# Performance work log

Measured on AMD Instinct MI355X. Metric: run time of the kernel, lower is better.

## Reference

```python
import jax, jax.numpy as jnp
import numpy as np

B, S, IN_DIM, P_DIM, H = 2, 2048, 1024, 512, 8
HD = P_DIM // H
N_PENTA = 1024
SCALES = (128, 256, 512)
K_NEIGH = max(16, min(int(S * 0.15), 128))  # adaptive window -> 128
SCALE = 1.0 / float(np.sqrt(HD))
EPS = 1e-5


def _ln(x, g, b):
    mu = jnp.mean(x, axis=-1, keepdims=True)
    var = jnp.mean((x - mu) ** 2, axis=-1, keepdims=True)
    return (x - mu) * jax.lax.rsqrt(var + EPS) * g + b


def setup_inputs() -> dict:
    key = jax.random.key(0)
    ks = list(jax.random.split(key, 6 + 2 * len(SCALES)))
    w = lambda k, shp: jax.random.normal(k, shp, jnp.float32) * 0.02
    inp = {
        'sequence_features': jax.random.normal(ks[0], (B, S, IN_DIM), jnp.float32),
        'shared_pentachora': jax.random.normal(ks[1], (N_PENTA, 5, P_DIM), jnp.float32),
        'shared_positions': jax.random.uniform(ks[2], (N_PENTA,), dtype=jnp.float32),
        'proj_W': w(ks[3], (IN_DIM, P_DIM)), 'proj_b': jnp.zeros((P_DIM,), jnp.float32),
        'ln_g': jnp.ones((P_DIM,), jnp.float32), 'ln_b': jnp.zeros((P_DIM,), jnp.float32),
        'qkv_W': w(ks[4], (P_DIM, 3 * P_DIM)), 'qkv_b': jnp.zeros((3 * P_DIM,), jnp.float32),
        'out_W': w(ks[5], (P_DIM, P_DIM)), 'out_b': jnp.zeros((P_DIM,), jnp.float32),
    }
    i = 6
    for s in SCALES:
        inp[f'w1_{s}'] = w(ks[i], (P_DIM, 2 * s)); inp[f'b1_{s}'] = jnp.zeros((2 * s,), jnp.float32)
        inp[f'g_{s}'] = jnp.ones((2 * s,), jnp.float32); inp[f'bb_{s}'] = jnp.zeros((2 * s,), jnp.float32)
        inp[f'w2_{s}'] = w(ks[i + 1], (2 * s, s)); inp[f'b2_{s}'] = jnp.zeros((s,), jnp.float32)
        i += 2
    return inp


def _attend_one(z_b, pos_b, qkv_W, qkv_b, out_W, out_b):
    # z_b: [S, P_DIM], pos_b: [S]
    qkv = (z_b @ qkv_W + qkv_b).reshape(S, 3, H, HD)
    q = jnp.transpose(qkv[:, 0], (1, 0, 2))  # [H, S, HD]
    k = jnp.transpose(qkv[:, 1], (1, 0, 2))
    v = jnp.transpose(qkv[:, 2], (1, 0, 2))
    dist = jnp.abs(pos_b[:, None] - pos_b[None, :])  # [S, S]
    _, routes = jax.lax.top_k(-dist, K_NEIGH)        # [S, K] nearest in Cantor space
    kg = k[:, routes, :]  # [H, S, K, HD] gathered keys
    vg = v[:, routes, :]
    scores = jnp.einsum('hqd,hqkd->hqk', q, kg) * SCALE
    attn = jax.nn.softmax(scores, axis=-1)
    out = jnp.einsum('hqk,hqkd->hqd', attn, vg)
    out = jnp.transpose(out, (1, 0, 2)).reshape(S, P_DIM)
    return out @ out_W + out_b


def reference(sequence_features, shared_pentachora, shared_positions, proj_W, proj_b, ln_g, ln_b, qkv_W, qkv_b, out_W, out_b, w1_128, b1_128, g_128, bb_128, w2_128, b2_128, w1_256, b1_256, g_256, bb_256, w2_256, b2_256, w1_512, b1_512, g_512, bb_512, w2_512, b2_512):
    # centroids from pentachora vertices, L2-normalized
    cent = shared_pentachora.mean(axis=1)
    cent = cent / jnp.clip(jnp.linalg.norm(cent, axis=-1, keepdims=True), 1e-12)
    # input projection -> LN -> GELU -> L2 normalize
    z = jax.nn.gelu(_ln(sequence_features @ proj_W + proj_b, ln_g, ln_b), approximate=False)
    z = z / jnp.clip(jnp.linalg.norm(z, axis=-1, keepdims=True), 1e-12)
    # match to opinion anchors, inherit Cantor positions
    anchor_ids = jnp.argmax(jnp.einsum('bnd,pd->bnp', z, cent), axis=-1)  # [B, S]
    cantor_positions = shared_positions[anchor_ids]  # [B, S]
    # per-sample geometric sparse attention (vmapped over batch)
    z_att = jax.vmap(_attend_one, in_axes=(0, 0, None, None, None, None))(
        z, cantor_positions, qkv_W, qkv_b, out_W, out_b)  # [B, S, P_DIM]
    pooled = z_att.mean(axis=1)  # [B, P_DIM] (no attention mask)
    scale_params = (
        (w1_128, b1_128, g_128, bb_128, w2_128, b2_128),
        (w1_256, b1_256, g_256, bb_256, w2_256, b2_256),
        (w1_512, b1_512, g_512, bb_512, w2_512, b2_512),
    )
    outs = []
    for (w1, b1, g, bb, w2, b2) in scale_params:
        h = jax.nn.gelu(_ln(pooled @ w1 + b1, g, bb), approximate=False)
        outs.append(h @ w2 + b2)
    return jnp.concatenate(outs, axis=-1)  # [B, 128+256+512] concatenated scale opinions
```

## Files before the change

kernel.cpp:

```cpp
#include <hip/hip_runtime.h>
#include <math.h>

#define DEV __device__ __forceinline__

static constexpr int S_LEN  = 2048;
static constexpr int IN_DIM = 1024;
static constexpr int P_DIM  = 512;
static constexpr int NHEAD  = 8;
static constexpr int HD     = 64;
static constexpr int KN     = 128;

typedef __attribute__((ext_vector_type(8))) short bf16x8;
typedef __attribute__((ext_vector_type(4))) float f32x4;

DEV float gelu_exact(float x) {
    return 0.5f * x * (1.0f + erff(x * 0.70710678118654752440f));
}

DEV short bf_hi(float x) {
    unsigned u = __float_as_uint(x);
    unsigned r = (u + 0x7fffu + ((u >> 16) & 1u)) >> 16;
    return (short)r;
}
DEV float bf_f(short h) { return __uint_as_float(((unsigned)(unsigned short)h) << 16); }

DEV float block_reduce_sum(float v, float* sm4) {
    #pragma unroll
    for (int off = 32; off; off >>= 1) v += __shfl_down(v, off, 64);
    int lane = threadIdx.x & 63, w = threadIdx.x >> 6;
    __syncthreads();
    if (lane == 0) sm4[w] = v;
    __syncthreads();
    return sm4[0] + sm4[1] + sm4[2] + sm4[3];
}

DEV float wave_sum(float v) {
    #pragma unroll
    for (int off = 32; off; off >>= 1) v += __shfl_xor(v, off, 64);
    return v;
}

DEV void wt_body(const float* __restrict__ W, short* __restrict__ WTh,
                 short* __restrict__ WTl, int K, int N, int bk, int bn,
                 float (*tile)[65]) {
    int t = threadIdx.x;
    int c = t & 63, r4 = t >> 6;
    #pragma unroll
    for (int i = 0; i < 16; i++) {
        int row = r4 + i * 4;
        tile[row][c] = W[(long)(bk * 64 + row) * N + bn * 64 + c];
    }
    __syncthreads();
    #pragma unroll
    for (int i = 0; i < 16; i++) {
        int n = r4 + i * 4;
        float v = tile[c][n];
        short h = bf_hi(v);
        long o = (long)(bn * 64 + n) * K + bk * 64 + c;
        WTh[o] = h;
        WTl[o] = bf_hi(v - bf_f(h));
    }
}

DEV void t32_body(const float* __restrict__ W, float* __restrict__ WT,
                  int K, int N, int bk, int bn, float (*tile)[65]) {
    int t = threadIdx.x;
    int c = t & 63, r4 = t >> 6;
    #pragma unroll
    for (int i = 0; i < 16; i++) {
        int row = r4 + i * 4;
        tile[row][c] = W[(long)(bk * 64 + row) * N + bn * 64 + c];
    }
    __syncthreads();
    #pragma unroll
    for (int i = 0; i < 16; i++) {
        int n = r4 + i * 4;
        WT[(long)(bn * 64 + n) * K + bk * 64 + c] = tile[c][n];
    }
}

__global__ __launch_bounds__(256) void k_prep(const float* __restrict__ penta,
                                              short* __restrict__ ch, short* __restrict__ cl,
                                              const float* __restrict__ projW,
                                              short* __restrict__ pjh, short* __restrict__ pjl,
                                              const float* __restrict__ qkvW,
                                              short* __restrict__ qkh, short* __restrict__ qkl,
                                              const float* __restrict__ seq,
                                              short* __restrict__ sh, short* __restrict__ sl,
                                              unsigned long long* __restrict__ rowkey,
                                              float* __restrict__ pooledZ,
                                              const float* __restrict__ outW, float* __restrict__ outWT,
                                              const float* __restrict__ w1_0,
                                              const float* __restrict__ w1_1,
                                              const float* __restrict__ w1_2, float* __restrict__ w1T,
                                              const float* __restrict__ w2_0,
                                              const float* __restrict__ w2_1,
                                              const float* __restrict__ w2_2, float* __restrict__ w2T) {
    __shared__ float tile[64][65];
    __shared__ float sm4[4];
    int blk = blockIdx.x, t = threadIdx.x;
    if (blk < 1024) {
        int p = blk;
        if (t < 4) rowkey[p * 4 + t] = 0ull;
        if (p < 4) pooledZ[p * 256 + t] = 0.f;
        float c0 = 0.f, c1 = 0.f;
        #pragma unroll
        for (int v = 0; v < 5; v++) {
            const float* row = penta + ((long)p * 5 + v) * P_DIM;
            c0 += row[t];
            c1 += row[t + 256];
        }
        c0 /= 5.0f; c1 /= 5.0f;
        float tot = block_reduce_sum(c0 * c0 + c1 * c1, sm4);
        float n = fmaxf(sqrtf(tot), 1e-12f);
        float v0 = c0 / n, v1 = c1 / n;
        short h0 = bf_hi(v0), h1 = bf_hi(v1);
        ch[p * P_DIM + t]       = h0;
        ch[p * P_DIM + t + 256] = h1;
        cl[p * P_DIM + t]       = bf_hi(v0 - bf_f(h0));
        cl[p * P_DIM + t + 256] = bf_hi(v1 - bf_f(h1));
    } else if (blk < 1152) {
        int id = blk - 1024;
        wt_body(projW, pjh, pjl, IN_DIM, P_DIM, id & 15, id >> 4, tile);
    } else if (blk < 1344) {
        int id = blk - 1152;
        wt_body(qkvW, qkh, qkl, P_DIM, 3 * P_DIM, id & 7, id >> 3, tile);
    } else if (blk < 2368) {
        long base = ((long)(blk - 1344) * 256 + t) * 16;
        #pragma unroll
        for (int u = 0; u < 4; u++) {
            float4 v = *(const float4*)(seq + base + u * 4);
            short h0 = bf_hi(v.x), h1 = bf_hi(v.y), h2 = bf_hi(v.z), h3 = bf_hi(v.w);
            *(short4*)(sh + base + u * 4) = make_short4(h0, h1, h2, h3);
            *(short4*)(sl + base + u * 4) =
                make_short4(bf_hi(v.x - bf_f(h0)), bf_hi(v.y - bf_f(h1)),
                            bf_hi(v.z - bf_f(h2)), bf_hi(v.w - bf_f(h3)));
        }
    } else if (blk < 2432) {
        int id = blk - 2368;
        t32_body(outW, outWT, 512, 512, id & 7, id >> 3, tile);
    } else if (blk < 2464) {
        int id = blk - 2432;
        t32_body(w1_0, w1T, 512, 256, id & 7, id >> 3, tile);
    } else if (blk < 2528) {
        int id = blk - 2464;
        t32_body(w1_1, w1T + 256 * 512, 512, 512, id & 7, id >> 3, tile);
    } else if (blk < 2656) {
        int id = blk - 2528;
        t32_body(w1_2, w1T + 768 * 512, 512, 1024, id & 7, id >> 3, tile);
    } else if (blk < 2664) {
        int id = blk - 2656;
        t32_body(w2_0, w2T, 256, 128, id & 3, id >> 2, tile);
    } else if (blk < 2696) {
        int id = blk - 2664;
        t32_body(w2_1, w2T + 32768, 512, 256, id & 7, id >> 3, tile);
    } else {
        int id = blk - 2696;
        t32_body(w2_2, w2T + 163840, 1024, 512, id & 15, id >> 4, tile);
    }
}

template <int BM, int K, int N, int EPI>
__global__ __launch_bounds__(256) void k_mm(const short* __restrict__ Ash,
                                            const short* __restrict__ Asl,
                                            const short* __restrict__ BTh,
                                            const short* __restrict__ BTl,
                                            const float* __restrict__ bias,
                                            float* __restrict__ C,
                                            unsigned long long* __restrict__ rowkey) {
    constexpr int TI  = BM / 32;
    constexpr int CA  = BM / 8;
    constexpr int NCH = 2 * CA + 32;
    __shared__ __align__(128) short AhS[BM * 64], AlS[BM * 64];
    __shared__ __align__(128) short BhS[128 * 64], BlS[128 * 64];
    int t = threadIdx.x;
    int lane = t & 63, wave = t >> 6;
    int wr = (wave >> 1) * (BM / 2), wc = (wave & 1) * 64;
    int m = lane & 15, quad = lane >> 4;
    int rb = blockIdx.x * BM, cb = blockIdx.y * 128;
    int r8 = lane >> 3, p8 = lane & 7;
    int sl = p8 ^ r8;

    f32x4 acc[TI][4];
    #pragma unroll
    for (int i = 0; i < TI; i++)
        #pragma unroll
        for (int j = 0; j < 4; j++) acc[i][j] = (f32x4){0.f, 0.f, 0.f, 0.f};

    for (int k0 = 0; k0 < K; k0 += 64) {
        __syncthreads();
        for (int c = wave; c < NCH; c += 4) {
            const short* src; short* dst;
            if (c < CA) {
                src = Ash + (long)(rb + c * 8 + r8) * K + k0 + sl * 8;
                dst = AhS + c * 512;
            } else if (c < 2 * CA) {
                int cc = c - CA;
                src = Asl + (long)(rb + cc * 8 + r8) * K + k0 + sl * 8;
                dst = AlS + cc * 512;
            } else if (c < 2 * CA + 16) {
                int cc = c - 2 * CA;
                src = BTh + (long)(cb + cc * 8 + r8) * K + k0 + sl * 8;
                dst = BhS + cc * 512;
            } else {
                int cc = c - 2 * CA - 16;
                src = BTl + (long)(cb + cc * 8 + r8) * K + k0 + sl * 8;
                dst = BlS + cc * 512;
            }
            __builtin_amdgcn_global_load_lds(
                (const __attribute__((address_space(1))) unsigned int*)src,
                (__attribute__((address_space(3))) unsigned int*)dst, 16, 0, 0);
        }
        __syncthreads();

        #pragma unroll
        for (int ks = 0; ks < 2; ks++) {
            int so = ((ks * 4 + quad) ^ (m & 7)) * 8;
            bf16x8 ah[TI], al[TI], bh[4], bl[4];
            #pragma unroll
            for (int i = 0; i < TI; i++) {
                int off = (wr + i * 16 + m) * 64 + so;
                ah[i] = *(const bf16x8*)(AhS + off);
                al[i] = *(const bf16x8*)(AlS + off);
            }
            #pragma unroll
            for (int j = 0; j < 4; j++) {
                int off = (wc + j * 16 + m) * 64 + so;
                bh[j] = *(const bf16x8*)(BhS + off);
                bl[j] = *(const bf16x8*)(BlS + off);
            }
            #pragma unroll
            for (int i = 0; i < TI; i++)
                #pragma unroll
                for (int j = 0; j < 4; j++) {
                    acc[i][j] = __builtin_amdgcn_mfma_f32_16x16x32_bf16(ah[i], bh[j], acc[i][j], 0, 0, 0);
                    acc[i][j] = __builtin_amdgcn_mfma_f32_16x16x32_bf16(ah[i], bl[j], acc[i][j], 0, 0, 0);
                    acc[i][j] = __builtin_amdgcn_mfma_f32_16x16x32_bf16(al[i], bh[j], acc[i][j], 0, 0, 0);
                }
        }
    }

    if (EPI == 0) {
        #pragma unroll
        for (int i = 0; i < TI; i++) {
            int gr0 = rb + wr + i * 16 + quad * 4;
            #pragma unroll
            for (int j = 0; j < 4; j++) {
                int gc = cb + wc + j * 16 + m;
                float bv = bias[gc];
                #pragma unroll
                for (int r = 0; r < 4; r++)
                    C[(long)(gr0 + r) * N + gc] = acc[i][j][r] + bv;
            }
        }
    } else {
        #pragma unroll
        for (int i = 0; i < TI; i++) {
            #pragma unroll
            for (int r = 0; r < 4; r++) {
                int gr = rb + wr + i * 16 + quad * 4 + r;
                float bv = acc[i][0][r];
                int bp = cb + wc + m;
                #pragma unroll
                for (int j = 1; j < 4; j++) {
                    float v = acc[i][j][r];
                    int p = cb + wc + j * 16 + m;
                    if (v > bv) { bv = v; bp = p; }
                }
                #pragma unroll
                for (int off = 1; off < 16; off <<= 1) {
                    float ov = __shfl_xor(bv, off, 64);
                    int op = __shfl_xor(bp, off, 64);
                    if (ov > bv || (ov == bv && op < bp)) { bv = ov; bp = op; }
                }
                if (m == 0) {
                    unsigned u = __float_as_uint(bv);
                    u = (u & 0x80000000u) ? ~u : (u | 0x80000000u);
                    unsigned long long key =
                        ((unsigned long long)u << 32) | (unsigned)(0xFFFFFFFFu - (unsigned)bp);
                    atomicMax(&rowkey[gr], key);
                }
            }
        }
    }
}

__global__ __launch_bounds__(256) void k_ln_gelu_norm(const float* __restrict__ Zin,
                                                      const float* __restrict__ g,
                                                      const float* __restrict__ b,
                                                      short* __restrict__ z_h,
                                                      short* __restrict__ z_l) {
    long row = blockIdx.x;
    int t = threadIdx.x;
    __shared__ float sm4[4];
    float x0 = Zin[row * P_DIM + t], x1 = Zin[row * P_DIM + t + 256];
    float mu = block_reduce_sum(x0 + x1, sm4) * (1.0f / P_DIM);
    float d0 = x0 - mu, d1 = x1 - mu;
    float var = block_reduce_sum(d0 * d0 + d1 * d1, sm4) * (1.0f / P_DIM);
    float rs = 1.0f / sqrtf(var + 1e-5f);
    float y0 = gelu_exact(d0 * rs * g[t] + b[t]);
    float y1 = gelu_exact(d1 * rs * g[t + 256] + b[t + 256]);
    float nn = block_reduce_sum(y0 * y0 + y1 * y1, sm4);
    float n = fmaxf(sqrtf(nn), 1e-12f);
    float v0 = y0 / n, v1 = y1 / n;
    short h0 = bf_hi(v0), h1 = bf_hi(v1);
    z_h[row * P_DIM + t]       = h0;
    z_h[row * P_DIM + t + 256] = h1;
    z_l[row * P_DIM + t]       = bf_hi(v0 - bf_f(h0));
    z_l[row * P_DIM + t + 256] = bf_hi(v1 - bf_f(h1));
}

__global__ __launch_bounds__(256) void k_rank(const unsigned long long* __restrict__ rowkey,
                                              const float* __restrict__ spos,
                                              int* __restrict__ order,
                                              float* __restrict__ pos_srt) {
    int b = blockIdx.y, t = threadIdx.x;
    __shared__ unsigned long long key[2048];
    for (int u = 0; u < 8; u++) {
        int i = t + u * 256;
        unsigned p = 0xFFFFFFFFu - (unsigned)(rowkey[b * 2048 + i] & 0xFFFFFFFFull);
        key[i] = (((unsigned long long)__float_as_uint(spos[p])) << 32) | (unsigned)i;
    }
    __syncthreads();
    int i = blockIdx.x * 256 + t;
    unsigned long long ki = key[i];
    int rank = 0;
    #pragma unroll 8
    for (int j = 0; j < 2048; j++) rank += (key[j] < ki) ? 1 : 0;
    order[b * 2048 + rank]   = i;
    pos_srt[b * 2048 + rank] = __uint_as_float((unsigned)(ki >> 32));
}

__global__ __launch_bounds__(256) void k_routes(const float* __restrict__ pos_srt,
                                                const int* __restrict__ order,
                                                unsigned long long* __restrict__ bmG,
                                                uint2* __restrict__ bounds) {
    int blk = blockIdx.x;
    int b = blk >> 9;
    int t = threadIdx.x;
    int lane = t & 63, wave = t >> 6;
    int r = (blk & 511) * 4 + wave;
    __shared__ float ps[2048];
    __shared__ unsigned short tk[2048];
    for (int u = 0; u < 8; u++) {
        int i = t + u * 256;
        ps[i] = pos_srt[b * 2048 + i];
        tk[i] = (unsigned short)order[b * 2048 + i];
    }
    __syncthreads();

    float pi = ps[r];
    float T = 3e38f;
    #pragma unroll
    for (int a2 = 0; a2 < 2; a2++) {
        int a = lane + a2 * 64;
        int jl = r - a, jr = r + 127 - a;
        if (jl >= 0 && jr <= 2047) {
            float dl = (a > 0)   ? (pi - ps[jl]) : 0.f;
            float dr = (a < 127) ? (ps[jr] - pi) : 0.f;
            T = fminf(T, fmaxf(dl, dr));
        }
    }
    #pragma unroll
    for (int off = 1; off < 64; off <<= 1) T = fminf(T, __shfl_xor(T, off, 64));

    int lo = 0, hi = r;
    while (lo < hi) { int mid = (lo + hi) >> 1; if (pi - ps[mid] <= T) hi = mid; else lo = mid + 1; }
    int mn = lo;
    lo = r; hi = 2047;
    while (lo < hi) { int mid = (lo + hi + 1) >> 1; if (ps[mid] - pi <= T) lo = mid; else hi = mid - 1; }
    int mx = lo;
    int Ls, Rs;
    if (T > 0.f) {
        lo = 0; hi = r;
        while (lo < hi) { int mid = (lo + hi) >> 1; if (pi - ps[mid] < T) hi = mid; else lo = mid + 1; }
        Ls = lo;
        lo = r; hi = 2047;
        while (lo < hi) { int mid = (lo + hi + 1) >> 1; if (ps[mid] - pi < T) lo = mid; else hi = mid - 1; }
        Rs = lo;
    } else { Ls = r + 1; Rs = r - 1; }

    int cnt_strict = (Rs >= Ls) ? (Rs - Ls + 1) : 0;
    int need = 128 - cnt_strict;
    int l0a, l0b, r0a, r0b;
    if (cnt_strict > 0) { l0a = mn; l0b = Ls - 1; r0a = Rs + 1; r0b = mx; }
    else                { l0a = mn; l0b = mx;     r0a = 1;      r0b = 0; }
    int nL = (l0b >= l0a) ? (l0b - l0a + 1) : 0;
    int nR = (r0b >= r0a) ? (r0b - r0a + 1) : 0;
    int tiecount = nL + nR;

    int X = 65535;
    if (need < tiecount) {
        int lo2 = 0, hi2 = 2047;
        while (lo2 < hi2) {
            int mid = (lo2 + hi2) >> 1;
            int cnt = 0;
            for (int e = lane; e < tiecount; e += 64) {
                int j = (e < nL) ? (l0a + e) : (r0a + e - nL);
                cnt += (tk[j] <= mid) ? 1 : 0;
            }
            #pragma unroll
            for (int off = 1; off < 64; off <<= 1) cnt += __shfl_xor(cnt, off, 64);
            if (cnt >= need) hi2 = mid; else lo2 = mid + 1;
        }
        X = lo2;
    }

    int qlo_loc = 1 << 30, qhi_loc = -1;
    if (lane < 32) {
        unsigned long long bits = 0;
        int j0 = lane << 6, j1 = j0 + 63;
        if (cnt_strict > 0) {
            int a0 = max(Ls, j0), a1 = min(Rs, j1);
            if (a0 <= a1) {
                int s = a0 - j0, e = a1 - j0;
                unsigned long long msk = (e - s == 63) ? ~0ull
                                       : (((1ull << (e - s + 1)) - 1) << s);
                bits |= msk;
            }
        }
        int a0 = max(l0a, j0), a1 = min(l0b, j1);
        for (int j = a0; j <= a1; j++) if (tk[j] <= X) bits |= 1ull << (j - j0);
        a0 = max(r0a, j0); a1 = min(r0b, j1);
        for (int j = a0; j <= a1; j++) if (tk[j] <= X) bits |= 1ull << (j - j0);
        if (bits) {
            qlo_loc = j0 + __builtin_ctzll(bits);
            qhi_loc = j0 + 63 - __builtin_clzll(bits);
        }
        bmG[((long)(b * 2048 + r)) * 32 + lane] = bits;
    }
    #pragma unroll
    for (int off = 1; off < 64; off <<= 1) {
        qlo_loc = min(qlo_loc, __shfl_xor(qlo_loc, off, 64));
        qhi_loc = max(qhi_loc, __shfl_xor(qhi_loc, off, 64));
    }
    if (lane == 0)
        bounds[b * 2048 + r] = make_uint2((unsigned)qlo_loc, (unsigned)qhi_loc);
}

__global__ __launch_bounds__(256) void k_kv(const float* __restrict__ qkv,
                                            const int* __restrict__ order,
                                            short* __restrict__ Ks_h,
                                            short* __restrict__ Ks_l,
                                            short* __restrict__ Vt_h) {
    __shared__ short tile[64][72];
    int blk = blockIdx.x, t = threadIdx.x;
    if (blk < 512) {
        int b = blk >> 8, bx = blk & 255;
        int lr = t >> 5;
        int seg = t & 31;
        int rank = bx * 8 + lr;
        int tok = order[b * 2048 + rank];
        const float4* src = (const float4*)qkv + (long)(b * 2048 + tok) * 384 + 128 + seg * 4;
        long dsto = (long)(b * 2048 + rank) * 512 + seg * 16;
        #pragma unroll
        for (int u = 0; u < 4; u++) {
            float4 v = src[u];
            short h0 = bf_hi(v.x), h1 = bf_hi(v.y), h2 = bf_hi(v.z), h3 = bf_hi(v.w);
            *(short4*)(Ks_h + dsto + u * 4) = make_short4(h0, h1, h2, h3);
            *(short4*)(Ks_l + dsto + u * 4) =
                make_short4(bf_hi(v.x - bf_f(h0)), bf_hi(v.y - bf_f(h1)),
                            bf_hi(v.z - bf_f(h2)), bf_hi(v.w - bf_f(h3)));
        }
    } else {
        int id = blk - 512;
        int rt = id & 31, dt = (id >> 5) & 7, b = id >> 8;
        int lr = t >> 2;
        int q4 = t & 3;
        int tok = order[b * 2048 + rt * 64 + lr];
        const float4* src = (const float4*)qkv + (long)(b * 2048 + tok) * 384 + 256 + dt * 16;
        #pragma unroll
        for (int u = 0; u < 4; u++) {
            float4 v = src[q4 + u * 4];
            int d0 = (q4 + u * 4) * 4;
            tile[d0 + 0][lr] = bf_hi(v.x);
            tile[d0 + 1][lr] = bf_hi(v.y);
            tile[d0 + 2][lr] = bf_hi(v.z);
            tile[d0 + 3][lr] = bf_hi(v.w);
        }
        __syncthreads();
        int d = t >> 2, c4 = t & 3;
        long o = ((long)(b * 512 + dt * 64 + d)) * 2048 + rt * 64 + c4 * 16;
        #pragma unroll
        for (int j = 0; j < 4; j++)
            *(short4*)(Vt_h + o + j * 4) = make_short4(tile[d][c4 * 16 + j * 4 + 0],
                                                       tile[d][c4 * 16 + j * 4 + 1],
                                                       tile[d][c4 * 16 + j * 4 + 2],
                                                       tile[d][c4 * 16 + j * 4 + 3]);
    }
}

__global__ __launch_bounds__(256) void k_attn(const float* __restrict__ qkv,
                                              const int* __restrict__ order,
                                              const unsigned long long* __restrict__ bmG,
                                              const uint2* __restrict__ bounds,
                                              const short* __restrict__ Ks_h,
                                              const short* __restrict__ Ks_l,
                                              const short* __restrict__ Vt_h,
                                              float* __restrict__ pooledZ) {
    __shared__ __align__(16) char smem[17280];
    short* Pt = (short*)smem;
    unsigned short* cm = (unsigned short*)(smem + 10240);
    float* Opart = (float*)smem;
    float2* ml = (float2*)(smem + 16384);
    int* sh_tok = (int*)(smem + 16896);
    int* sh_lohi = (int*)(smem + 16960);
    float2* sc = (float2*)(smem + 16968);

    int gb = blockIdx.x;
    int b  = gb >> 9;
    int qg = (gb >> 2) & 127;
    int hp = gb & 3;
    int h0 = hp * 2;
    int r0 = qg * 16;
    int t = threadIdx.x;
    int lane = t & 63, wave = t >> 6;
    int rh = wave & 1, hs = wave >> 1;
    int key = lane & 15, quad = lane >> 4;

    const float4* qkvF4 = (const float4*)qkv;

    if (t < 16) sh_tok[t] = order[b * 2048 + r0 + t];
    if (t == 0) { sh_lohi[0] = 1 << 30; sh_lohi[1] = 0; }
    #pragma unroll
    for (int u = 0; u < 8; u++) {
        int e = t + u * 256;
        int c = e >> 4, q = e & 15;
        cm[c * 16 + q] = (unsigned short)(
            (bmG[((long)(b * 2048 + r0 + q)) * 32 + (c >> 2)] >> ((c & 3) * 16)) & 0xFFFF);
    }
    __syncthreads();
    if (t < 16) {
        uint2 bd = bounds[b * 2048 + r0 + t];
        atomicMin(&sh_lohi[0], (int)bd.x);
        atomicMax(&sh_lohi[1], (int)bd.y);
    }

    bf16x8 qh[2], ql[2];
    {
        long tq = (long)(b * 2048 + sh_tok[key]) * 384;
        #pragma unroll
        for (int ks = 0; ks < 2; ks++) {
            float4 v0 = qkvF4[tq + (h0 + hs) * 16 + ks * 8 + quad * 2];
            float4 v1 = qkvF4[tq + (h0 + hs) * 16 + ks * 8 + quad * 2 + 1];
            float vv[8] = {v0.x, v0.y, v0.z, v0.w, v1.x, v1.y, v1.z, v1.w};
            #pragma unroll
            for (int j = 0; j < 8; j++) {
                short hb = bf_hi(vv[j]);
                qh[ks][j] = hb;
                ql[ks][j] = bf_hi(vv[j] - bf_f(hb));
            }
        }
    }
    __syncthreads();
    int lo = sh_lohi[0] & ~63, hi = sh_lohi[1] + 1;

    float mrow[4], lrow[4];
    f32x4 Ont[4];
    #pragma unroll
    for (int r = 0; r < 4; r++) { mrow[r] = -1e30f; lrow[r] = 0.f; }
    #pragma unroll
    for (int nt = 0; nt < 4; nt++) Ont[nt] = (f32x4){0.f, 0.f, 0.f, 0.f};

    short* PtH = Pt + wave * 1280;
    short* PtL = PtH + 640;

    int hd = h0 + hs;
    long kbase = ((long)b * 2048) * 512 + hd * 64 + quad * 8;
    long vbase = ((long)(b * 512 + hd * 64 + key)) * 2048;

    for (int c0 = lo; c0 < hi; c0 += 64) {
        int cb = c0 + rh * 32;
        if (cb >= hi) continue;
        int ch0 = cb >> 4;
        unsigned long long m0 = *(const unsigned long long*)(cm + ch0 * 16 + quad * 4);
        unsigned long long m1 = (ch0 + 1 < 128)
            ? *(const unsigned long long*)(cm + (ch0 + 1) * 16 + quad * 4) : 0ull;
        if (!__any((m0 | m1) != 0ull)) continue;

        long kr0 = kbase + (long)(cb + key) * 512;
        long kr1 = kbase + (long)(cb + 16 + key) * 512;

        f32x4 S0 = (f32x4){0.f,0.f,0.f,0.f}, S1 = (f32x4){0.f,0.f,0.f,0.f};
        #pragma unroll
        for (int ks = 0; ks < 2; ks++) {
            bf16x8 b0h = *(const bf16x8*)(Ks_h + kr0 + ks * 32);
            bf16x8 b0l = *(const bf16x8*)(Ks_l + kr0 + ks * 32);
            bf16x8 b1h = *(const bf16x8*)(Ks_h + kr1 + ks * 32);
            bf16x8 b1l = *(const bf16x8*)(Ks_l + kr1 + ks * 32);
            S0 = __builtin_amdgcn_mfma_f32_16x16x32_bf16(qh[ks], b0h, S0, 0, 0, 0);
            S0 = __builtin_amdgcn_mfma_f32_16x16x32_bf16(qh[ks], b0l, S0, 0, 0, 0);
            S0 = __builtin_amdgcn_mfma_f32_16x16x32_bf16(ql[ks], b0h, S0, 0, 0, 0);
            S1 = __builtin_amdgcn_mfma_f32_16x16x32_bf16(qh[ks], b1h, S1, 0, 0, 0);
            S1 = __builtin_amdgcn_mfma_f32_16x16x32_bf16(qh[ks], b1l, S1, 0, 0, 0);
            S1 = __builtin_amdgcn_mfma_f32_16x16x32_bf16(ql[ks], b1h, S1, 0, 0, 0);
        }
        float s0[4], s1[4], p0[4], p1[4];
        unsigned bit0[4], bit1[4];
        #pragma unroll
        for (int r = 0; r < 4; r++) {
            bit0[r] = (unsigned)((m0 >> (r * 16 + key)) & 1);
            bit1[r] = (unsigned)((m1 >> (r * 16 + key)) & 1);
            s0[r] = bit0[r] ? S0[r] * 0.125f : -1e30f;
            s1[r] = bit1[r] ? S1[r] * 0.125f : -1e30f;
        }
        #pragma unroll
        for (int r = 0; r < 4; r++) {
            float cmax = fmaxf(s0[r], s1[r]);
            cmax = fmaxf(cmax, __shfl_xor(cmax, 1, 64));
            cmax = fmaxf(cmax, __shfl_xor(cmax, 2, 64));
            cmax = fmaxf(cmax, __shfl_xor(cmax, 4, 64));
            cmax = fmaxf(cmax, __shfl_xor(cmax, 8, 64));
            float mn = fmaxf(mrow[r], cmax);
            float alpha = __expf(mrow[r] - mn);
            mrow[r] = mn;
            p0[r] = bit0[r] ? __expf(s0[r] - mn) : 0.f;
            p1[r] = bit1[r] ? __expf(s1[r] - mn) : 0.f;
            float rs = p0[r] + p1[r];
            rs += __shfl_xor(rs, 1, 64);
            rs += __shfl_xor(rs, 2, 64);
            rs += __shfl_xor(rs, 4, 64);
            rs += __shfl_xor(rs, 8, 64);
            lrow[r] = lrow[r] * alpha + rs;
            #pragma unroll
            for (int nt = 0; nt < 4; nt++) Ont[nt][r] *= alpha;
        }
        #pragma unroll
        for (int r = 0; r < 4; r++) {
            short ha = bf_hi(p0[r]);
            PtH[(quad * 4 + r) * 40 + key] = ha;
            PtL[(quad * 4 + r) * 40 + key] = bf_hi(p0[r] - bf_f(ha));
            short hb = bf_hi(p1[r]);
            PtH[(quad * 4 + r) * 40 + 16 + key] = hb;
            PtL[(quad * 4 + r) * 40 + 16 + key] = bf_hi(p1[r] - bf_f(hb));
        }
        bf16x8 pfh = *(const bf16x8*)(PtH + key * 40 + quad * 8);
        bf16x8 pfl = *(const bf16x8*)(PtL + key * 40 + quad * 8);
        #pragma unroll
        for (int nt = 0; nt < 4; nt++) {
            bf16x8 vf = *(const bf16x8*)(Vt_h + vbase + (long)nt * 16 * 2048
                                         + cb + quad * 8);
            Ont[nt] = __builtin_amdgcn_mfma_f32_16x16x32_bf16(pfh, vf, Ont[nt], 0, 0, 0);
            Ont[nt] = __builtin_amdgcn_mfma_f32_16x16x32_bf16(pfl, vf, Ont[nt], 0, 0, 0);
        }
    }

    if (key == 0) {
        #pragma unroll
        for (int r = 0; r < 4; r++)
            ml[(rh * 2 + hs) * 16 + quad * 4 + r] = make_float2(mrow[r], lrow[r]);
    }
    __syncthreads();
    #pragma unroll
    for (int nt = 0; nt < 4; nt++)
        #pragma unroll
        for (int r = 0; r < 4; r++)
            Opart[rh * 2048 + (quad * 4 + r) * 128 + hs * 64 + nt * 16 + key] = Ont[nt][r];

    if (t < 32) {
        int q = t >> 1, hs2 = t & 1;
        float2 a = ml[(0 * 2 + hs2) * 16 + q];
        float2 c = ml[(1 * 2 + hs2) * 16 + q];
        float M = fmaxf(a.x, c.x);
        float w0 = __expf(a.x - M), w1 = __expf(c.x - M);
        float inv = 1.0f / fmaxf(a.y * w0 + c.y * w1, 1e-37f);
        sc[hs2 * 16 + q] = make_float2(w0 * inv, w1 * inv);
    }
    __syncthreads();

    if (t < 128) {
        int d = t, hs2 = d >> 6;
        float s = 0.f;
        #pragma unroll
        for (int q = 0; q < 16; q++) {
            float2 w = sc[hs2 * 16 + q];
            s += Opart[q * 128 + d] * w.x + Opart[2048 + q * 128 + d] * w.y;
        }
        atomicAdd(&pooledZ[b * P_DIM + h0 * HD + d], s);
    }
}

__global__ __launch_bounds__(256) void k_gemv_opool(const float* __restrict__ pooledZ,
                                                    const float* __restrict__ outWT,
                                                    const float* __restrict__ outb,
                                                    float* __restrict__ pooled) {
    int b = blockIdx.y, t = threadIdx.x;
    int lane = t & 63, w = t >> 6;
    __shared__ float pz[P_DIM];
    pz[t]       = pooledZ[b * P_DIM + t];
    pz[t + 256] = pooledZ[b * P_DIM + t + 256];
    __syncthreads();
    int c = blockIdx.x * 4 + w;
    const float* wp = outWT + (long)c * 512;
    float acc = 0.f;
    #pragma unroll
    for (int i = 0; i < 8; i++) acc = fmaf(pz[lane + i * 64], wp[lane + i * 64], acc);
    acc = wave_sum(acc);
    if (lane == 0) pooled[b * P_DIM + c] = acc + (float)S_LEN * outb[c];
}

__global__ __launch_bounds__(256) void k_gemv_fc1(const float* __restrict__ pooled,
                                                  const float* __restrict__ w1T,
                                                  const float* __restrict__ b1_0,
                                                  const float* __restrict__ b1_1,
                                                  const float* __restrict__ b1_2,
                                                  float* __restrict__ h) {
    int b = blockIdx.y, t = threadIdx.x;
    int lane = t & 63, w = t >> 6;
    __shared__ float pl[P_DIM];
    pl[t]       = pooled[b * P_DIM + t]       * (1.0f / S_LEN);
    pl[t + 256] = pooled[b * P_DIM + t + 256] * (1.0f / S_LEN);
    __syncthreads();
    int c = blockIdx.x * 4 + w;
    const float* wp = w1T + (long)c * 512;
    float acc = 0.f;
    #pragma unroll
    for (int i = 0; i < 8; i++) acc = fmaf(pl[lane + i * 64], wp[lane + i * 64], acc);
    acc = wave_sum(acc);
    if (lane == 0) {
        float bb = (c < 256) ? b1_0[c] : (c < 768) ? b1_1[c - 256] : b1_2[c - 768];
        h[(long)b * 1792 + c] = acc + bb;
    }
}

__global__ __launch_bounds__(256) void k_gemv_fc2(const float* __restrict__ h,
                                                  const float* __restrict__ w2T,
                                                  const float* __restrict__ b2_0,
                                                  const float* __restrict__ b2_1,
                                                  const float* __restrict__ b2_2,
                                                  float* __restrict__ out) {
    int b = blockIdx.y, t = threadIdx.x;
    int lane = t & 63, w = t >> 6;
    __shared__ float hh[1792];
    for (int u = 0; u < 7; u++) hh[t + u * 256] = h[(long)b * 1792 + t + u * 256];
    __syncthreads();
    int c = blockIdx.x * 4 + w;
    const float* wp; const float* hp; int s2; float bb;
    if (c < 128)      { wp = w2T + (long)c * 256;                hp = hh;       s2 = 256;  bb = b2_0[c]; }
    else if (c < 384) { wp = w2T + 32768 + (long)(c - 128) * 512;  hp = hh + 256; s2 = 512;  bb = b2_1[c - 128]; }
    else              { wp = w2T + 163840 + (long)(c - 384) * 1024; hp = hh + 768; s2 = 1024; bb = b2_2[c - 384]; }
    float acc = 0.f;
    for (int i = lane; i < s2; i += 64) acc = fmaf(hp[i], wp[i], acc);
    acc = wave_sum(acc);
    if (lane == 0) out[b * 896 + c] = acc + bb;
}

__global__ __launch_bounds__(256) void k_exp_ln(float* __restrict__ h,
                                                const float* __restrict__ g0, const float* __restrict__ bb0,
                                                const float* __restrict__ g1, const float* __restrict__ bb1,
                                                const float* __restrict__ g2, const float* __restrict__ bb2) {
    int e = blockIdx.x, b = blockIdx.y, t = threadIdx.x;
    __shared__ float sm4[4];
    const int offs[3] = {0, 256, 768};
    const int ns[3]   = {256, 512, 1024};
    const float* gs[3]  = {g0, g1, g2};
    const float* bbs[3] = {bb0, bb1, bb2};
    int n = ns[e];
    float* hp = h + (long)b * 1792 + offs[e];
    const float* g = gs[e]; const float* bb = bbs[e];

    float x[4];
    float loc = 0.f;
    for (int u = 0; u < 4; u++) {
        int j = t + u * 256;
        x[u] = (j < n) ? hp[j] : 0.f;
        loc += x[u];
    }
    float mu = block_reduce_sum(loc, sm4) / (float)n;
    loc = 0.f;
    for (int u = 0; u < 4; u++) {
        int j = t + u * 256;
        if (j < n) { float d = x[u] - mu; loc += d * d; }
    }
    float var = block_reduce_sum(loc, sm4) / (float)n;
    float rs = 1.0f / sqrtf(var + 1e-5f);
    for (int u = 0; u < 4; u++) {
        int j = t + u * 256;
        if (j < n) hp[j] = gelu_exact((x[u] - mu) * rs * g[j] + bb[j]);
    }
}

extern "C" void kernel_launch(void* const* d_in, const int* in_sizes, int n_in,
                              void* d_out, int out_size, void* d_ws, size_t ws_size,
                              hipStream_t stream) {
    const float* seq   = (const float*)d_in[0];
    const float* penta = (const float*)d_in[1];
    const float* spos  = (const float*)d_in[2];
    const float* projW = (const float*)d_in[3];
    const float* projb = (const float*)d_in[4];
    const float* lng   = (const float*)d_in[5];
    const float* lnb   = (const float*)d_in[6];
    const float* qkvW  = (const float*)d_in[7];
    const float* qkvb  = (const float*)d_in[8];
    const float* outW  = (const float*)d_in[9];
    const float* outb  = (const float*)d_in[10];

    float* ws      = (float*)d_ws;
    float* z_pre   = ws;
    short* z_h     = (short*)(z_pre + 2097152);
    short* z_l     = z_h + 2097152;
    float* qkv     = (float*)(z_l + 2097152);
    float* pooledZ = qkv + 6291456;
    float* pooled  = pooledZ + 4096;
    float* hbuf    = pooled + 1024;
    unsigned long long* rowkey = (unsigned long long*)(hbuf + 4096);
    float* pos_srt = (float*)(rowkey + 4096);
    int*   order   = (int*)(pos_srt + 4096);
    uint2* bounds  = (uint2*)(order + 4096);
    unsigned long long* bmG = (unsigned long long*)(bounds + 4096);
    short* cent_h  = (short*)(bmG + 131072);
    short* cent_l  = cent_h + 524288;
    short* pjWT_h  = cent_l + 524288;
    short* pjWT_l  = pjWT_h + 524288;
    short* qkWT_h  = pjWT_l + 524288;
    short* qkWT_l  = qkWT_h + 786432;
    float* outWT   = (float*)(qkWT_l + 786432);
    float* w1T     = outWT + 262144;
    float* w2T     = w1T + 917504;

    short* seq_h = (short*)qkv;
    short* seq_l = seq_h + 4194304;
    short* Ks_h = (short*)z_pre;
    short* Ks_l = Ks_h + 2097152;
    short* Vt_h = cent_h;

    k_prep<<<2824, 256, 0, stream>>>(penta, cent_h, cent_l,
                                     projW, pjWT_h, pjWT_l,
                                     qkvW, qkWT_h, qkWT_l,
                                     seq, seq_h, seq_l,
                                     rowkey, pooledZ,
                                     outW, outWT,
                                     (const float*)d_in[11],
                                     (const float*)d_in[17],
                                     (const float*)d_in[23], w1T,
                                     (const float*)d_in[15],
                                     (const float*)d_in[21],
                                     (const float*)d_in[27], w2T);

    { dim3 g(64, 4);  k_mm<64, IN_DIM, P_DIM, 0><<<g, 256, 0, stream>>>(
          seq_h, seq_l, pjWT_h, pjWT_l, projb, z_pre, nullptr); }
    k_ln_gelu_norm<<<4096, 256, 0, stream>>>(z_pre, lng, lnb, z_h, z_l);

    { dim3 g(32, 8);  k_mm<128, P_DIM, 1024, 1><<<g, 256, 0, stream>>>(
          z_h, z_l, cent_h, cent_l, nullptr, nullptr, rowkey); }
    { dim3 g(8, 2);   k_rank<<<g, 256, 0, stream>>>(rowkey, spos, order, pos_srt); }

    { dim3 g(32, 12); k_mm<128, P_DIM, 3 * P_DIM, 0><<<g, 256, 0, stream>>>(
          z_h, z_l, qkWT_h, qkWT_l, qkvb, qkv, nullptr); }
    k_routes<<<1024, 256, 0, stream>>>(pos_srt, order, bmG, bounds);
    k_kv<<<1024, 256, 0, stream>>>(qkv, order, Ks_h, Ks_l, Vt_h);
    k_attn<<<1024, 256, 0, stream>>>(qkv, order, bmG, bounds,
                                     Ks_h, Ks_l, Vt_h, pooledZ);

    { dim3 g(128, 2); k_gemv_opool<<<g, 256, 0, stream>>>(pooledZ, outWT, outb, pooled); }
    { dim3 g(448, 2); k_gemv_fc1<<<g, 256, 0, stream>>>(pooled, w1T,
        (const float*)d_in[12], (const float*)d_in[18], (const float*)d_in[24], hbuf); }
    { dim3 g(3, 2);   k_exp_ln<<<g, 256, 0, stream>>>(hbuf,
        (const float*)d_in[13], (const float*)d_in[14],
        (const float*)d_in[19], (const float*)d_in[20],
        (const float*)d_in[25], (const float*)d_in[26]); }
    { dim3 g(224, 2); k_gemv_fc2<<<g, 256, 0, stream>>>(hbuf, w2T,
        (const float*)d_in[16], (const float*)d_in[22], (const float*)d_in[28],
        (float*)d_out); }
}
```

Before: 332.6 us.

## Merge anchor and QKV GEMMs into one launch, fuse routes with KV prep

Replaces the separate anchor-matching GEMM and QKV GEMM with a single kernel whose grid's y dimension selects between centroid argmax and QKV output. It also merges route-bitmask construction with K/V conversion into one launch with a shared LDS buffer. Wave priority is raised around the MFMA blocks in attention. The goal is fewer launches and better GPU fill, since the independent pieces now run concurrently. The cost is extra branching and larger per-block shared memory in the merged kernels.

```diff
diff --git a/kernel.cpp b/kernel.cpp
--- a/kernel.cpp
+++ b/kernel.cpp
@@ -285,6 +285,137 @@
     }
 }
 
+__global__ __launch_bounds__(256) void k_mmz(const short* __restrict__ Ash,
+                                             const short* __restrict__ Asl,
+                                             const short* __restrict__ Ch,
+                                             const short* __restrict__ Cl,
+                                             const short* __restrict__ Qh,
+                                             const short* __restrict__ Ql,
+                                             const float* __restrict__ bias,
+                                             float* __restrict__ C,
+                                             unsigned long long* __restrict__ rowkey) {
+    constexpr int BM = 128, K = 512;
+    constexpr int TI  = BM / 32;
+    constexpr int CA  = BM / 8;
+    constexpr int NCH = 2 * CA + 32;
+    __shared__ __align__(128) short AhS[BM * 64], AlS[BM * 64];
+    __shared__ __align__(128) short BhS[128 * 64], BlS[128 * 64];
+    int t = threadIdx.x;
+    int lane = t & 63, wave = t >> 6;
+    int wr = (wave >> 1) * (BM / 2), wc = (wave & 1) * 64;
+    int m = lane & 15, quad = lane >> 4;
+    bool anchor = blockIdx.y < 8;
+    const short* BTh = anchor ? Ch : Qh;
+    const short* BTl = anchor ? Cl : Ql;
+    int rb = blockIdx.x * BM;
+    int cb = (anchor ? blockIdx.y : (blockIdx.y - 8)) * 128;
+    int r8 = lane >> 3, p8 = lane & 7;
+    int sl = p8 ^ r8;
+
+    f32x4 acc[TI][4];
+    #pragma unroll
+    for (int i = 0; i < TI; i++)
+        #pragma unroll
+        for (int j = 0; j < 4; j++) acc[i][j] = (f32x4){0.f, 0.f, 0.f, 0.f};
+
+    for (int k0 = 0; k0 < K; k0 += 64) {
+        __syncthreads();
+        for (int c = wave; c < NCH; c += 4) {
+            const short* src; short* dst;
+            if (c < CA) {
+                src = Ash + (long)(rb + c * 8 + r8) * K + k0 + sl * 8;
+                dst = AhS + c * 512;
+            } else if (c < 2 * CA) {
+                int cc = c - CA;
+                src = Asl + (long)(rb + cc * 8 + r8) * K + k0 + sl * 8;
+                dst = AlS + cc * 512;
+            } else if (c < 2 * CA + 16) {
+                int cc = c - 2 * CA;
+                src = BTh + (long)(cb + cc * 8 + r8) * K + k0 + sl * 8;
+                dst = BhS + cc * 512;
+            } else {
+                int cc = c - 2 * CA - 16;
+                src = BTl + (long)(cb + cc * 8 + r8) * K + k0 + sl * 8;
+                dst = BlS + cc * 512;
+            }
+            __builtin_amdgcn_global_load_lds(
+                (const __attribute__((address_space(1))) unsigned int*)src,
+                (__attribute__((address_space(3))) unsigned int*)dst, 16, 0, 0);
+        }
+        __syncthreads();
+
+        #pragma unroll
+        for (int ks = 0; ks < 2; ks++) {
+            int so = ((ks * 4 + quad) ^ (m & 7)) * 8;
+            bf16x8 ah[TI], al[TI], bh[4], bl[4];
+            #pragma unroll
+            for (int i = 0; i < TI; i++) {
+                int off = (wr + i * 16 + m) * 64 + so;
+                ah[i] = *(const bf16x8*)(AhS + off);
+                al[i] = *(const bf16x8*)(AlS + off);
+            }
+            #pragma unroll
+            for (int j = 0; j < 4; j++) {
+                int off = (wc + j * 16 + m) * 64 + so;
+                bh[j] = *(const bf16x8*)(BhS + off);
+                bl[j] = *(const bf16x8*)(BlS + off);
+            }
+            #pragma unroll
+            for (int i = 0; i < TI; i++)
+                #pragma unroll
+                for (int j = 0; j < 4; j++) {
+                    acc[i][j] = __builtin_amdgcn_mfma_f32_16x16x32_bf16(ah[i], bh[j], acc[i][j], 0, 0, 0);
+                    acc[i][j] = __builtin_amdgcn_mfma_f32_16x16x32_bf16(ah[i], bl[j], acc[i][j], 0, 0, 0);
+                    acc[i][j] = __builtin_amdgcn_mfma_f32_16x16x32_bf16(al[i], bh[j], acc[i][j], 0, 0, 0);
+                }
+        }
+    }
+
+    if (!anchor) {
+        #pragma unroll
+        for (int i = 0; i < TI; i++) {
+            int gr0 = rb + wr + i * 16 + quad * 4;
+            #pragma unroll
+            for (int j = 0; j < 4; j++) {
+                int gc = cb + wc + j * 16 + m;
+                float bv = bias[gc];
+                #pragma unroll
+                for (int r = 0; r < 4; r++)
+                    C[(long)(gr0 + r) * 1536 + gc] = acc[i][j][r] + bv;
+            }
+        }
+    } else {
+        #pragma unroll
+        for (int i = 0; i < TI; i++) {
+            #pragma unroll
+            for (int r = 0; r < 4; r++) {
+                int gr = rb + wr + i * 16 + quad * 4 + r;
+                float bv = acc[i][0][r];
+                int bp = cb + wc + m;
+                #pragma unroll
+                for (int j = 1; j < 4; j++) {
+                    float v = acc[i][j][r];
+                    int p = cb + wc + j * 16 + m;
+                    if (v > bv) { bv = v; bp = p; }
+                }
+                #pragma unroll
+                for (int off = 1; off < 16; off <<= 1) {
+                    float ov = __shfl_xor(bv, off, 64);
+                    int op = __shfl_xor(bp, off, 64);
+                    if (ov > bv || (ov == bv && op < bp)) { bv = ov; bp = op; }
+                }
+                if (m == 0) {
+                    unsigned u = __float_as_uint(bv);
+                    u = (u & 0x80000000u) ? ~u : (u | 0x80000000u);
+                    unsigned long long key =
+                        ((unsigned long long)u << 32) | (unsigned)(0xFFFFFFFFu - (unsigned)bp);
+                    atomicMax(&rowkey[gr], key);
+                }
+            }
+        }
+    }
+}
+
 __global__ __launch_bounds__(256) void k_ln_gelu_norm(const float* __restrict__ Zin,
                                                       const float* __restrict__ g,
                                                       const float* __restrict__ b,
@@ -331,121 +462,119 @@
     pos_srt[b * 2048 + rank] = __uint_as_float((unsigned)(ki >> 32));
 }
 
-__global__ __launch_bounds__(256) void k_routes(const float* __restrict__ pos_srt,
-                                                const int* __restrict__ order,
-                                                unsigned long long* __restrict__ bmG,
-                                                uint2* __restrict__ bounds) {
-    int blk = blockIdx.x;
-    int b = blk >> 9;
-    int t = threadIdx.x;
-    int lane = t & 63, wave = t >> 6;
-    int r = (blk & 511) * 4 + wave;
-    __shared__ float ps[2048];
-    __shared__ unsigned short tk[2048];
-    for (int u = 0; u < 8; u++) {
-        int i = t + u * 256;
-        ps[i] = pos_srt[b * 2048 + i];
-        tk[i] = (unsigned short)order[b * 2048 + i];
-    }
-    __syncthreads();
-
-    float pi = ps[r];
-    float T = 3e38f;
-    #pragma unroll
-    for (int a2 = 0; a2 < 2; a2++) {
-        int a = lane + a2 * 64;
-        int jl = r - a, jr = r + 127 - a;
-        if (jl >= 0 && jr <= 2047) {
-            float dl = (a > 0)   ? (pi - ps[jl]) : 0.f;
-            float dr = (a < 127) ? (ps[jr] - pi) : 0.f;
-            T = fminf(T, fmaxf(dl, dr));
-        }
-    }
-    #pragma unroll
-    for (int off = 1; off < 64; off <<= 1) T = fminf(T, __shfl_xor(T, off, 64));
-
-    int lo = 0, hi = r;
-    while (lo < hi) { int mid = (lo + hi) >> 1; if (pi - ps[mid] <= T) hi = mid; else lo = mid + 1; }
-    int mn = lo;
-    lo = r; hi = 2047;
-    while (lo < hi) { int mid = (lo + hi + 1) >> 1; if (ps[mid] - pi <= T) lo = mid; else hi = mid - 1; }
-    int mx = lo;
-    int Ls, Rs;
-    if (T > 0.f) {
-        lo = 0; hi = r;
-        while (lo < hi) { int mid = (lo + hi) >> 1; if (pi - ps[mid] < T) hi = mid; else lo = mid + 1; }
-        Ls = lo;
+__global__ __launch_bounds__(256) void k_routeskv(const float* __restrict__ pos_srt,
+                                                  const int* __restrict__ order,
+                                                  unsigned long long* __restrict__ bmG,
+                                                  uint2* __restrict__ bounds,
+                                                  const float* __restrict__ qkv,
+                                                  short* __restrict__ Ks_h,
+                                                  short* __restrict__ Ks_l,
+                                                  short* __restrict__ Vt_h) {
+    __shared__ __align__(16) char smem[12288];
+    int blk0 = blockIdx.x, t = threadIdx.x;
+    if (blk0 < 1024) {
+        float* ps = (float*)smem;
+        unsigned short* tk = (unsigned short*)(smem + 8192);
+        int blk = blk0;
+        int b = blk >> 9;
+        int lane = t & 63, wave = t >> 6;
+        int r = (blk & 511) * 4 + wave;
+        for (int u = 0; u < 8; u++) {
+            int i = t + u * 256;
+            ps[i] = pos_srt[b * 2048 + i];
+            tk[i] = (unsigned short)order[b * 2048 + i];
+        }
+        __syncthreads();
+
+        float pi = ps[r];
+        float T = 3e38f;
+        #pragma unroll
+        for (int a2 = 0; a2 < 2; a2++) {
+            int a = lane + a2 * 64;
+            int jl = r - a, jr = r + 127 - a;
+            if (jl >= 0 && jr <= 2047) {
+                float dl = (a > 0)   ? (pi - ps[jl]) : 0.f;
+                float dr = (a < 127) ? (ps[jr] - pi) : 0.f;
+                T = fminf(T, fmaxf(dl, dr));
+            }
+        }
+        #pragma unroll
+        for (int off = 1; off < 64; off <<= 1) T = fminf(T, __shfl_xor(T, off, 64));
+
+        int lo = 0, hi = r;
+        while (lo < hi) { int mid = (lo + hi) >> 1; if (pi - ps[mid] <= T) hi = mid; else lo = mid + 1; }
+        int mn = lo;
         lo = r; hi = 2047;
-        while (lo < hi) { int mid = (lo + hi + 1) >> 1; if (ps[mid] - pi < T) lo = mid; else hi = mid - 1; }
-        Rs = lo;
-    } else { Ls = r + 1; Rs = r - 1; }
-
-    int cnt_strict = (Rs >= Ls) ? (Rs - Ls + 1) : 0;
-    int need = 128 - cnt_strict;
-    int l0a, l0b, r0a, r0b;
-    if (cnt_strict > 0) { l0a = mn; l0b = Ls - 1; r0a = Rs + 1; r0b = mx; }
-    else                { l0a = mn; l0b = mx;     r0a = 1;      r0b = 0; }
-    int nL = (l0b >= l0a) ? (l0b - l0a + 1) : 0;
-    int nR = (r0b >= r0a) ? (r0b - r0a + 1) : 0;
-    int tiecount = nL + nR;
-
-    int X = 65535;
-    if (need < tiecount) {
-        int lo2 = 0, hi2 = 2047;
-        while (lo2 < hi2) {
-            int mid = (lo2 + hi2) >> 1;
-            int cnt = 0;
-            for (int e = lane; e < tiecount; e += 64) {
-                int j = (e < nL) ? (l0a + e) : (r0a + e - nL);
-                cnt += (tk[j] <= mid) ? 1 : 0;
-            }
-            #pragma unroll
-            for (int off = 1; off < 64; off <<= 1) cnt += __shfl_xor(cnt, off, 64);
-            if (cnt >= need) hi2 = mid; else lo2 = mid + 1;
-        }
-        X = lo2;
-    }
-
-    int qlo_loc = 1 << 30, qhi_loc = -1;
-    if (lane < 32) {
-        unsigned long long bits = 0;
-        int j0 = lane << 6, j1 = j0 + 63;
-        if (cnt_strict > 0) {
-            int a0 = max(Ls, j0), a1 = min(Rs, j1);
-            if (a0 <= a1) {
-                int s = a0 - j0, e = a1 - j0;
-                unsigned long long msk = (e - s == 63) ? ~0ull
-                                       : (((1ull << (e - s + 1)) - 1) << s);
-                bits |= msk;
-            }
-        }
-        int a0 = max(l0a, j0), a1 = min(l0b, j1);
-        for (int j = a0; j <= a1; j++) if (tk[j] <= X) bits |= 1ull << (j - j0);
-        a0 = max(r0a, j0); a1 = min(r0b, j1);
-        for (int j = a0; j <= a1; j++) if (tk[j] <= X) bits |= 1ull << (j - j0);
-        if (bits) {
-            qlo_loc = j0 + __builtin_ctzll(bits);
-            qhi_loc = j0 + 63 - __builtin_clzll(bits);
-        }
-        bmG[((long)(b * 2048 + r)) * 32 + lane] = bits;
-    }
-    #pragma unroll
-    for (int off = 1; off < 64; off <<= 1) {
-        qlo_loc = min(qlo_loc, __shfl_xor(qlo_loc, off, 64));
-        qhi_loc = max(qhi_loc, __shfl_xor(qhi_loc, off, 64));
-    }
-    if (lane == 0)
-        bounds[b * 2048 + r] = make_uint2((unsigned)qlo_loc, (unsigned)qhi_loc);
-}
-
-__global__ __launch_bounds__(256) void k_kv(const float* __restrict__ qkv,
-                                            const int* __restrict__ order,
-                                            short* __restrict__ Ks_h,
-                                            short* __restrict__ Ks_l,
-                                            short* __restrict__ Vt_h) {
-    __shared__ short tile[64][72];
-    int blk = blockIdx.x, t = threadIdx.x;
-    if (blk < 512) {
+        while (lo < hi) { int mid = (lo + hi + 1) >> 1; if (ps[mid] - pi <= T) lo = mid; else hi = mid - 1; }
+        int mx = lo;
+        int Ls, Rs;
+        if (T > 0.f) {
+            lo = 0; hi = r;
+            while (lo < hi) { int mid = (lo + hi) >> 1; if (pi - ps[mid] < T) hi = mid; else lo = mid + 1; }
+            Ls = lo;
+            lo = r; hi = 2047;
+            while (lo < hi) { int mid = (lo + hi + 1) >> 1; if (ps[mid] - pi < T) lo = mid; else hi = mid - 1; }
+            Rs = lo;
+        } else { Ls = r + 1; Rs = r - 1; }
+
+        int cnt_strict = (Rs >= Ls) ? (Rs - Ls + 1) : 0;
+        int need = 128 - cnt_strict;
+        int l0a, l0b, r0a, r0b;
+        if (cnt_strict > 0) { l0a = mn; l0b = Ls - 1; r0a = Rs + 1; r0b = mx; }
+        else                { l0a = mn; l0b = mx;     r0a = 1;      r0b = 0; }
+        int nL = (l0b >= l0a) ? (l0b - l0a + 1) : 0;
+        int nR = (r0b >= r0a) ? (r0b - r0a + 1) : 0;
+        int tiecount = nL + nR;
+
+        int X = 65535;
+        if (need < tiecount) {
+            int lo2 = 0, hi2 = 2047;
+            while (lo2 < hi2) {
+                int mid = (lo2 + hi2) >> 1;
+                int cnt = 0;
+                for (int e = lane; e < tiecount; e += 64) {
+                    int j = (e < nL) ? (l0a + e) : (r0a + e - nL);
+                    cnt += (tk[j] <= mid) ? 1 : 0;
+                }
+                #pragma unroll
+                for (int off = 1; off < 64; off <<= 1) cnt += __shfl_xor(cnt, off, 64);
+                if (cnt >= need) hi2 = mid; else lo2 = mid + 1;
+            }
+            X = lo2;
+        }
+
+        int qlo_loc = 1 << 30, qhi_loc = -1;
+        if (lane < 32) {
+            unsigned long long bits = 0;
+            int j0 = lane << 6, j1 = j0 + 63;
+            if (cnt_strict > 0) {
+                int a0 = max(Ls, j0), a1 = min(Rs, j1);
+                if (a0 <= a1) {
+                    int s = a0 - j0, e = a1 - j0;
+                    unsigned long long msk = (e - s == 63) ? ~0ull
+                                           : (((1ull << (e - s + 1)) - 1) << s);
+                    bits |= msk;
+                }
+            }
+            int a0 = max(l0a, j0), a1 = min(l0b, j1);
+            for (int j = a0; j <= a1; j++) if (tk[j] <= X) bits |= 1ull << (j - j0);
+            a0 = max(r0a, j0); a1 = min(r0b, j1);
+            for (int j = a0; j <= a1; j++) if (tk[j] <= X) bits |= 1ull << (j - j0);
+            if (bits) {
+                qlo_loc = j0 + __builtin_ctzll(bits);
+                qhi_loc = j0 + 63 - __builtin_clzll(bits);
+            }
+            bmG[((long)(b * 2048 + r)) * 32 + lane] = bits;
+        }
+        #pragma unroll
+        for (int off = 1; off < 64; off <<= 1) {
+            qlo_loc = min(qlo_loc, __shfl_xor(qlo_loc, off, 64));
+            qhi_loc = max(qhi_loc, __shfl_xor(qhi_loc, off, 64));
+        }
+        if (lane == 0)
+            bounds[b * 2048 + r] = make_uint2((unsigned)qlo_loc, (unsigned)qhi_loc);
+    } else if (blk0 < 1536) {
+        int blk = blk0 - 1024;
         int b = blk >> 8, bx = blk & 255;
         int lr = t >> 5;
         int seg = t & 31;
@@ -463,7 +592,8 @@
                             bf_hi(v.z - bf_f(h2)), bf_hi(v.w - bf_f(h3)));
         }
     } else {
-        int id = blk - 512;
+        short (*tile)[72] = (short(*)[72])smem;
+        int id = blk0 - 1536;
         int rt = id & 31, dt = (id >> 5) & 7, b = id >> 8;
         int lr = t >> 2;
         int q4 = t & 3;
@@ -582,6 +712,7 @@
         long kr1 = kbase + (long)(cb + 16 + key) * 512;
 
         f32x4 S0 = (f32x4){0.f,0.f,0.f,0.f}, S1 = (f32x4){0.f,0.f,0.f,0.f};
+        __builtin_amdgcn_s_setprio(1);
         #pragma unroll
         for (int ks = 0; ks < 2; ks++) {
             bf16x8 b0h = *(const bf16x8*)(Ks_h + kr0 + ks * 32);
@@ -595,6 +726,7 @@
             S1 = __builtin_amdgcn_mfma_f32_16x16x32_bf16(qh[ks], b1l, S1, 0, 0, 0);
             S1 = __builtin_amdgcn_mfma_f32_16x16x32_bf16(ql[ks], b1h, S1, 0, 0, 0);
         }
+        __builtin_amdgcn_s_setprio(0);
         float s0[4], s1[4], p0[4], p1[4];
         unsigned bit0[4], bit1[4];
         #pragma unroll
@@ -636,6 +768,7 @@
         }
         bf16x8 pfh = *(const bf16x8*)(PtH + key * 40 + quad * 8);
         bf16x8 pfl = *(const bf16x8*)(PtL + key * 40 + quad * 8);
+        __builtin_amdgcn_s_setprio(1);
         #pragma unroll
         for (int nt = 0; nt < 4; nt++) {
             bf16x8 vf = *(const bf16x8*)(Vt_h + vbase + (long)nt * 16 * 2048
@@ -643,6 +776,7 @@
             Ont[nt] = __builtin_amdgcn_mfma_f32_16x16x32_bf16(pfh, vf, Ont[nt], 0, 0, 0);
             Ont[nt] = __builtin_amdgcn_mfma_f32_16x16x32_bf16(pfl, vf, Ont[nt], 0, 0, 0);
         }
+        __builtin_amdgcn_s_setprio(0);
     }
 
     if (key == 0) {
@@ -841,14 +975,12 @@
           seq_h, seq_l, pjWT_h, pjWT_l, projb, z_pre, nullptr); }
     k_ln_gelu_norm<<<4096, 256, 0, stream>>>(z_pre, lng, lnb, z_h, z_l);
 
-    { dim3 g(32, 8);  k_mm<128, P_DIM, 1024, 1><<<g, 256, 0, stream>>>(
-          z_h, z_l, cent_h, cent_l, nullptr, nullptr, rowkey); }
+    { dim3 g(32, 20); k_mmz<<<g, 256, 0, stream>>>(
+          z_h, z_l, cent_h, cent_l, qkWT_h, qkWT_l, qkvb, qkv, rowkey); }
+
     { dim3 g(8, 2);   k_rank<<<g, 256, 0, stream>>>(rowkey, spos, order, pos_srt); }
-
-    { dim3 g(32, 12); k_mm<128, P_DIM, 3 * P_DIM, 0><<<g, 256, 0, stream>>>(
-          z_h, z_l, qkWT_h, qkWT_l, qkvb, qkv, nullptr); }
-    k_routes<<<1024, 256, 0, stream>>>(pos_srt, order, bmG, bounds);
-    k_kv<<<1024, 256, 0, stream>>>(qkv, order, Ks_h, Ks_l, Vt_h);
+    k_routeskv<<<2048, 256, 0, stream>>>(pos_srt, order, bmG, bounds,
+                                         qkv, Ks_h, Ks_l, Vt_h);
     k_attn<<<1024, 256, 0, stream>>>(qkv, order, bmG, bounds,
                                      Ks_h, Ks_l, Vt_h, pooledZ);
 
```

New measurement: 329.2 us. No clear change (-1.0%).
